# Performance work log

Measured on AMD Instinct MI355X. Metric: run time of the kernel, lower is better.

The kernel has to match this reference:

```python
import jax, jax.numpy as jnp
import numpy as np

H = 12          # num_heads
EPS = 1e-10
DELU_P = 10.0


def delu(x):
    # delu_feature_map: param*relu(x) + (exp(param*min(x,0)) - 1) + 1
    pos = jax.nn.relu(x)
    neg = x - pos
    return DELU_P * pos + jnp.exp(DELU_P * neg)


def setup_inputs() -> dict:
    key = jax.random.key(0)
    ks = jax.random.split(key, 7)
    B, N, C = 4, 4096, 768
    x = jax.random.normal(ks[0], (B, N, C), dtype=jnp.float32)
    y = jax.random.normal(ks[1], (B, N, C), dtype=jnp.float32)
    qkv_w = jax.random.normal(ks[2], (3 * C, C), dtype=jnp.float32) * 0.02
    proj1_w = jax.random.normal(ks[3], (C, C), dtype=jnp.float32) * 0.02
    proj1_b = jnp.zeros((C,), dtype=jnp.float32)
    proj2_w = jax.random.normal(ks[4], (C, C), dtype=jnp.float32) * 0.02
    proj2_b = jnp.zeros((C,), dtype=jnp.float32)
    return {"x": x, "y": y, "qkv_w": qkv_w, "proj1_w": proj1_w,
            "proj1_b": proj1_b, "proj2_w": proj2_w, "proj2_b": proj2_b}


def reference(x, y, qkv_w, proj1_w, proj1_b, proj2_w, proj2_b):
    B, N, C = x.shape
    D = C // H
    scale = D ** (-0.5)

    qkv = (x @ qkv_w.T).reshape(B, N, 3, H, D).transpose(2, 0, 3, 1, 4)
    q, k, v = qkv[0], qkv[1], qkv[2]              # (B,H,N,D) each
    l_k = y.reshape(B, N, H, D).transpose(0, 2, 1, 3)  # (B,H,N,D)

    q = delu(q)
    k = delu(k)
    l_k = delu(l_k)

    # torch.einsum('bhnc,bhcc,bhn->bhnc', q, kv, norm) uses only diag(kv);
    # diag(k^T @ v) = sum_n k*v elementwise -> compute diagonals directly.
    kv_diag = jnp.einsum('bhnc,bhnc->bhc', k, v) * scale      # (B,H,D)
    l_kv_diag = jnp.einsum('bhnc,bhnc->bhc', l_k, v) * scale  # (B,H,D)

    k_sum = k.sum(axis=-2) + EPS                               # (B,H,D)
    norm = 1.0 / jnp.einsum('bhnc,bhc->bhn', q, k_sum)         # (B,H,N)

    attn_local = q * kv_diag[:, :, None, :] * norm[..., None]   # (B,H,N,D)
    attn_global = q * l_kv_diag[:, :, None, :] * norm[..., None]

    xo = attn_local.transpose(0, 2, 1, 3).reshape(B, N, C)
    yo = attn_global.transpose(0, 2, 1, 3).reshape(B, N, C)
    xo = xo @ proj1_w.T + proj1_b
    yo = yo @ proj2_w.T + proj2_b
    return (xo, yo)
```

## Files before the change

kernel.cpp:

```cpp
#include <hip/hip_runtime.h>
#include <hip/hip_bf16.h>

typedef unsigned short u16;
typedef unsigned int u32;
typedef __bf16 bf16x8 __attribute__((ext_vector_type(8)));
typedef float f32x4 __attribute__((ext_vector_type(4)));

__device__ __forceinline__ float bf2f(u16 u) {
    u32 x = ((u32)u) << 16;
    return __builtin_bit_cast(float, x);
}
__device__ __forceinline__ u16 f2bf(float f) {
    u32 x = __builtin_bit_cast(u32, f);
    u32 r = (x + 0x7fffu + ((x >> 16) & 1u)) >> 16;
    return (u16)r;
}
__device__ __forceinline__ float delu(float x) {
    return x > 0.f ? fmaf(10.f, x, 1.f) : __expf(10.f * x);
}

__global__ __launch_bounds__(256) void convert_all(
    const float4* __restrict__ x, const float4* __restrict__ wq,
    u16* __restrict__ xb, u16* __restrict__ wqb, float* __restrict__ red)
{
    const int NX = 3145728, NQ = 442368;
    int gid = blockIdx.x * blockDim.x + threadIdx.x;
    if (gid < 9216) red[gid] = 0.f;
    int stride = gridDim.x * blockDim.x;
    for (int i = gid; i < NX + NQ; i += stride) {
        const float4* src; u16* dst; int li;
        if (i < NX) { src = x;  dst = xb;  li = i; }
        else        { src = wq; dst = wqb; li = i - NX; }
        float4 f = src[li];
        ushort4 u;
        u.x = f2bf(f.x); u.y = f2bf(f.y); u.z = f2bf(f.z); u.w = f2bf(f.w);
        *(ushort4*)&dst[4 * (size_t)li] = u;
    }
}

__device__ __forceinline__ void gemm_core(
    const u16* __restrict__ A, const u16* __restrict__ Bt,
    int K, int m0, int n0, u16* ldsA, u16* ldsB, f32x4 acc[4][4])
{
    const int tid  = threadIdx.x;
    const int lane = tid & 63;
    const int wave = tid >> 6;
    const int wm = wave >> 1, wn = wave & 1;
    const int quad = lane >> 4, r = lane & 15;

    for (int kt = 0; kt < K; kt += 32) {
#pragma unroll
        for (int it = 0; it < 2; ++it) {
            int c   = wave + 4 * it;
            int q_  = c >> 1;
            int row = ((c & 1) << 6) + lane;
            const u16* ga = A  + (size_t)(m0 + row) * K + kt + q_ * 8;
            const u16* gb = Bt + (size_t)(n0 + row) * K + kt + q_ * 8;
            __builtin_amdgcn_global_load_lds(
                (const __attribute__((address_space(1))) u32*)(const void*)ga,
                (__attribute__((address_space(3))) u32*)(void*)&ldsA[c * 512], 16, 0, 0);
            __builtin_amdgcn_global_load_lds(
                (const __attribute__((address_space(1))) u32*)(const void*)gb,
                (__attribute__((address_space(3))) u32*)(void*)&ldsB[c * 512], 16, 0, 0);
        }
        __syncthreads();
        bf16x8 af[4], bfr[4];
#pragma unroll
        for (int i = 0; i < 4; ++i)
            af[i] = *(const bf16x8*)&ldsA[quad * 1024 + (wm * 64 + i * 16 + r) * 8];
#pragma unroll
        for (int j = 0; j < 4; ++j)
            bfr[j] = *(const bf16x8*)&ldsB[quad * 1024 + (wn * 64 + j * 16 + r) * 8];
#pragma unroll
        for (int i = 0; i < 4; ++i)
#pragma unroll
            for (int j = 0; j < 4; ++j)
                acc[i][j] = __builtin_amdgcn_mfma_f32_16x16x32_bf16(
                    af[i], bfr[j], acc[i][j], 0, 0, 0);
        __syncthreads();
    }
}

__global__ __launch_bounds__(256) void gemm_qkv(
    const u16* __restrict__ A, const u16* __restrict__ Bt, u16* __restrict__ C)
{
    const int l = blockIdx.x;
    const int xcd = l & 7, s = l >> 3;
    const int ml = s & 15, nt = s >> 4;
    const int m0 = (xcd * 16 + ml) * 128, n0 = nt * 128;

    __shared__ u16 ldsA[4096], ldsB[4096];
    f32x4 acc[4][4] = {};
    gemm_core(A, Bt, 768, m0, n0, ldsA, ldsB, acc);

    const int lane = threadIdx.x & 63;
    const int wave = threadIdx.x >> 6;
    const int wm = wave >> 1, wn = wave & 1;
    const int l15 = lane & 15, l4 = lane >> 4;
#pragma unroll
    for (int i = 0; i < 4; ++i) {
#pragma unroll
        for (int j = 0; j < 4; ++j) {
            int col = n0 + wn * 64 + j * 16 + l15;
            int row = m0 + wm * 64 + i * 16 + l4 * 4;
            bool isqk = col < 1536;
#pragma unroll
            for (int rr = 0; rr < 4; ++rr) {
                float v = acc[i][j][rr];
                if (isqk) v = delu(v);
                C[(size_t)(row + rr) * 2304 + col] = f2bf(v);
            }
        }
    }
}

__global__ __launch_bounds__(256) void reduce_kv(
    const u16* __restrict__ qkv, const float* __restrict__ y,
    float* __restrict__ ksum, float* __restrict__ kvd, float* __restrict__ lkvd)
{
    int blk = blockIdx.x;
    int b = blk / 192, rem = blk % 192;
    int h = rem >> 4, chunk = rem & 15;
    int t = threadIdx.x;
    int d2 = t & 31, sub = t >> 5;
    int col = h * 64 + 2 * d2;

    float s_k0 = 0, s_k1 = 0, s_kv0 = 0, s_kv1 = 0, s_l0 = 0, s_l1 = 0;
    for (int i = 0; i < 32; ++i) {
        int n = chunk * 256 + sub + 8 * i;
        size_t row = (size_t)(b << 12) + n;
        u32 kk = *(const u32*)&qkv[row * 2304 + 768 + col];
        u32 vv = *(const u32*)&qkv[row * 2304 + 1536 + col];
        float2 yy = *(const float2*)&y[row * 768 + col];
        float k0 = bf2f((u16)(kk & 0xffff)), k1 = bf2f((u16)(kk >> 16));
        float v0 = bf2f((u16)(vv & 0xffff)), v1 = bf2f((u16)(vv >> 16));
        float l0 = delu(yy.x), l1 = delu(yy.y);
        s_k0 += k0;                       s_k1 += k1;
        s_kv0 = fmaf(k0, v0, s_kv0);      s_kv1 = fmaf(k1, v1, s_kv1);
        s_l0  = fmaf(l0, v0, s_l0);       s_l1  = fmaf(l1, v1, s_l1);
    }
    __shared__ float red[256][6];
    red[t][0] = s_k0; red[t][1] = s_k1; red[t][2] = s_kv0;
    red[t][3] = s_kv1; red[t][4] = s_l0; red[t][5] = s_l1;
    __syncthreads();
    if (t < 32) {
        float a0 = red[t][0], a1 = red[t][1], a2 = red[t][2];
        float a3 = red[t][3], a4 = red[t][4], a5 = red[t][5];
        for (int s = 1; s < 8; ++s) {
            a0 += red[t + 32 * s][0]; a1 += red[t + 32 * s][1];
            a2 += red[t + 32 * s][2]; a3 += red[t + 32 * s][3];
            a4 += red[t + 32 * s][4]; a5 += red[t + 32 * s][5];
        }
        int bh = b * 12 + h;
        int d = 2 * t;
        atomicAdd(&ksum[bh * 64 + d],     a0);
        atomicAdd(&ksum[bh * 64 + d + 1], a1);
        atomicAdd(&kvd[bh * 64 + d],      a2 * 0.125f);
        atomicAdd(&kvd[bh * 64 + d + 1],  a3 * 0.125f);
        atomicAdd(&lkvd[bh * 64 + d],     a4 * 0.125f);
        atomicAdd(&lkvd[bh * 64 + d + 1], a5 * 0.125f);
    }
}

__global__ __launch_bounds__(256) void scale_weights(
    const float* __restrict__ w1, const float* __restrict__ w2,
    const float* __restrict__ kvd, const float* __restrict__ lkvd,
    u16* __restrict__ w1s, u16* __restrict__ w2s)
{
    const int NITEM = 1179648;
    int gid = blockIdx.x * blockDim.x + threadIdx.x;
    int stride = gridDim.x * blockDim.x;
    for (int i = gid; i < NITEM; i += stride) {
        int t = i / 589824, r = i % 589824;
        int b = r / 147456, rr = r % 147456;
        int o = rr / 192, c = (rr % 192) * 4;
        const float* w = t ? w2 : w1;
        const float* dg = t ? lkvd : kvd;
        u16* dst = t ? w2s : w1s;
        float4 wf = *(const float4*)&w[o * 768 + c];
        float4 sf = *(const float4*)&dg[(b * 12 + (c >> 6)) * 64 + (c & 63)];
        ushort4 u;
        u.x = f2bf(wf.x * sf.x); u.y = f2bf(wf.y * sf.y);
        u.z = f2bf(wf.z * sf.z); u.w = f2bf(wf.w * sf.w);
        *(ushort4*)&dst[(size_t)b * 589824 + o * 768 + c] = u;
    }
}

__global__ __launch_bounds__(768) void norm_q(
    const u16* __restrict__ qkv, const float* __restrict__ ksum,
    u16* __restrict__ qn)
{
    int row = blockIdx.x;
    int c = threadIdx.x;
    int h = c >> 6, d = c & 63;
    int b = row >> 12;
    int bh = b * 12 + h;
    float qf = bf2f(qkv[(size_t)row * 2304 + c]);
    float ks = ksum[bh * 64 + d] + 1e-10f;
    float p = qf * ks;
#pragma unroll
    for (int off = 32; off; off >>= 1) p += __shfl_xor(p, off);
    qn[(size_t)row * 768 + c] = f2bf(qf / p);
}

__global__ __launch_bounds__(256) void gemm_proj(
    const u16* __restrict__ A,
    const u16* __restrict__ W1s, const float* __restrict__ b1, float* __restrict__ O1,
    const u16* __restrict__ W2s, const float* __restrict__ b2, float* __restrict__ O2)
{
    const int l = blockIdx.x;
    const int xcd = l & 7, s = l >> 3;
    const int ml = s & 15, c_ = s >> 4;
    const int nt = c_ % 6, z = c_ / 6;
    const int m0 = (xcd * 16 + ml) * 128, n0 = nt * 128;
    const int b = m0 >> 12;
    const u16* W = (z ? W2s : W1s) + (size_t)b * 589824;
    const float* bias = z ? b2 : b1;
    float* O = z ? O2 : O1;

    __shared__ u16 ldsA[4096], ldsB[4096];
    f32x4 acc[4][4] = {};
    gemm_core(A, W, 768, m0, n0, ldsA, ldsB, acc);

    const int lane = threadIdx.x & 63;
    const int wave = threadIdx.x >> 6;
    const int wm = wave >> 1, wn = wave & 1;
    const int l15 = lane & 15, l4 = lane >> 4;
#pragma unroll
    for (int i = 0; i < 4; ++i) {
#pragma unroll
        for (int j = 0; j < 4; ++j) {
            int col = n0 + wn * 64 + j * 16 + l15;
            int row = m0 + wm * 64 + i * 16 + l4 * 4;
            float bv = bias[col];
#pragma unroll
            for (int rr = 0; rr < 4; ++rr)
                O[(size_t)(row + rr) * 768 + col] = acc[i][j][rr] + bv;
        }
    }
}

extern "C" void kernel_launch(void* const* d_in, const int* in_sizes, int n_in,
                              void* d_out, int out_size, void* d_ws, size_t ws_size,
                              hipStream_t stream)
{
    const float* x     = (const float*)d_in[0];
    const float* y     = (const float*)d_in[1];
    const float* qkv_w = (const float*)d_in[2];
    const float* w1    = (const float*)d_in[3];
    const float* b1    = (const float*)d_in[4];
    const float* w2    = (const float*)d_in[5];
    const float* b2    = (const float*)d_in[6];
    float* out = (float*)d_out;

    char* ws = (char*)d_ws;
    u16* xb   = (u16*)(ws);
    u16* wqb  = (u16*)(ws + 25165824);
    u16* w1s  = (u16*)(ws + 25165824);
    u16* w2s  = (u16*)(ws + 29884416);
    float* red  = (float*)(ws + 34603008);
    float* ksum = red;
    float* kvd  = red + 3072;
    float* lkvd = red + 6144;
    u16* qkvb = (u16*)d_out;
    u16* qn   = xb;

    convert_all<<<4096, 256, 0, stream>>>(
        (const float4*)x, (const float4*)qkv_w, xb, wqb, red);

    gemm_qkv<<<2304, 256, 0, stream>>>(xb, wqb, qkvb);

    reduce_kv<<<768, 256, 0, stream>>>(qkvb, y, ksum, kvd, lkvd);

    scale_weights<<<1152, 256, 0, stream>>>(w1, w2, kvd, lkvd, w1s, w2s);

    norm_q<<<16384, 768, 0, stream>>>(qkvb, ksum, qn);

    gemm_proj<<<1536, 256, 0, stream>>>(
        qn, w1s, b1, out, w2s, b2, out + 12582912);
}
```

Measured before the change: 434.5 us.

## Triple-buffer LDS tiles in GEMM core to overlap global loads with MFMA

Replaces the single-buffered load-sync-compute-sync GEMM loop with a three-stage LDS ring. Tile loads are issued two steps ahead through global_load_lds, and explicit vmcnt waits plus one barrier per step replace the two __syncthreads. The aim is to hide global memory latency behind MFMA work in both the QKV and projection GEMMs. In exchange, LDS use per block triples (to 48 KB), which may lower occupancy, and the correctness of the hand-written waitcnt depends on each thread issuing exactly four loads per tile.

```diff
diff --git a/kernel.cpp b/kernel.cpp
--- a/kernel.cpp
+++ b/kernel.cpp
@@ -38,7 +38,8 @@
     }
 }
 
-__device__ __forceinline__ void gemm_core(
+template<int TILES>
+__device__ __forceinline__ void gemm_core_pipe(
     const u16* __restrict__ A, const u16* __restrict__ Bt,
     int K, int m0, int n0, u16* ldsA, u16* ldsB, f32x4 acc[4][4])
 {
@@ -48,36 +49,52 @@
     const int wm = wave >> 1, wn = wave & 1;
     const int quad = lane >> 4, r = lane & 15;
 
-    for (int kt = 0; kt < K; kt += 32) {
+    auto issue = [&](int t, int buf) {
 #pragma unroll
         for (int it = 0; it < 2; ++it) {
             int c   = wave + 4 * it;
             int q_  = c >> 1;
             int row = ((c & 1) << 6) + lane;
-            const u16* ga = A  + (size_t)(m0 + row) * K + kt + q_ * 8;
-            const u16* gb = Bt + (size_t)(n0 + row) * K + kt + q_ * 8;
+            const u16* ga = A  + (size_t)(m0 + row) * K + t * 32 + q_ * 8;
+            const u16* gb = Bt + (size_t)(n0 + row) * K + t * 32 + q_ * 8;
             __builtin_amdgcn_global_load_lds(
                 (const __attribute__((address_space(1))) u32*)(const void*)ga,
-                (__attribute__((address_space(3))) u32*)(void*)&ldsA[c * 512], 16, 0, 0);
+                (__attribute__((address_space(3))) u32*)(void*)&ldsA[buf * 4096 + c * 512],
+                16, 0, 0);
             __builtin_amdgcn_global_load_lds(
                 (const __attribute__((address_space(1))) u32*)(const void*)gb,
-                (__attribute__((address_space(3))) u32*)(void*)&ldsB[c * 512], 16, 0, 0);
-        }
-        __syncthreads();
+                (__attribute__((address_space(3))) u32*)(void*)&ldsB[buf * 4096 + c * 512],
+                16, 0, 0);
+        }
+    };
+    auto compute = [&](int buf) {
         bf16x8 af[4], bfr[4];
 #pragma unroll
         for (int i = 0; i < 4; ++i)
-            af[i] = *(const bf16x8*)&ldsA[quad * 1024 + (wm * 64 + i * 16 + r) * 8];
+            af[i] = *(const bf16x8*)&ldsA[buf * 4096 + quad * 1024 + (wm * 64 + i * 16 + r) * 8];
 #pragma unroll
         for (int j = 0; j < 4; ++j)
-            bfr[j] = *(const bf16x8*)&ldsB[quad * 1024 + (wn * 64 + j * 16 + r) * 8];
+            bfr[j] = *(const bf16x8*)&ldsB[buf * 4096 + quad * 1024 + (wn * 64 + j * 16 + r) * 8];
 #pragma unroll
         for (int i = 0; i < 4; ++i)
 #pragma unroll
             for (int j = 0; j < 4; ++j)
                 acc[i][j] = __builtin_amdgcn_mfma_f32_16x16x32_bf16(
                     af[i], bfr[j], acc[i][j], 0, 0, 0);
-        __syncthreads();
+    };
+
+    issue(0, 0);
+    issue(1, 1);
+#pragma unroll
+    for (int t = 0; t < TILES; ++t) {
+        if (t + 1 < TILES) {
+            asm volatile("s_waitcnt vmcnt(4)" ::: "memory");
+        } else {
+            asm volatile("s_waitcnt vmcnt(0)" ::: "memory");
+        }
+        asm volatile("s_barrier" ::: "memory");
+        if (t + 2 < TILES) issue(t + 2, (t + 2) % 3);
+        compute(t % 3);
     }
 }
 
@@ -89,9 +106,9 @@
     const int ml = s & 15, nt = s >> 4;
     const int m0 = (xcd * 16 + ml) * 128, n0 = nt * 128;
 
-    __shared__ u16 ldsA[4096], ldsB[4096];
+    __shared__ u16 ldsA[12288], ldsB[12288];
     f32x4 acc[4][4] = {};
-    gemm_core(A, Bt, 768, m0, n0, ldsA, ldsB, acc);
+    gemm_core_pipe<24>(A, Bt, 768, m0, n0, ldsA, ldsB, acc);
 
     const int lane = threadIdx.x & 63;
     const int wave = threadIdx.x >> 6;
@@ -218,9 +235,9 @@
     const float* bias = z ? b2 : b1;
     float* O = z ? O2 : O1;
 
-    __shared__ u16 ldsA[4096], ldsB[4096];
+    __shared__ u16 ldsA[12288], ldsB[12288];
     f32x4 acc[4][4] = {};
-    gemm_core(A, W, 768, m0, n0, ldsA, ldsB, acc);
+    gemm_core_pipe<24>(A, W, 768, m0, n0, ldsA, ldsB, acc);
 
     const int lane = threadIdx.x & 63;
     const int wave = threadIdx.x >> 6;
```

Result: slower. 443.6 us (+2.1%).
